# Kernel tuning notes

Measured on AMD Instinct MI355X. Metric: run time of the kernel, lower is better.

## Reference

```python
import jax, jax.numpy as jnp
import numpy as np

HIST, CNTX, PRED = 336, 168, 24
C = 1            # c_in == c_out == 1 (univariate)
HID = 128        # GRU hidden size
NFEAT = 5        # hourly time features (freq_map['H'])
EMB = 10 * NFEAT # embedding_dim * freq_map['H'] = 50
NLAGS = HIST - CNTX            # 168 lag taps
IN_DIM = EMB + NLAGS           # rnn input size = 218
NSAMP = 8192     # num_parallel_samples


def setup_inputs() -> dict:
    key = jax.random.key(0)
    ks = jax.random.split(key, 8)
    s = lambda fan: 1.0 / np.sqrt(fan)
    return {
        "x": jax.random.normal(ks[0], (1, HIST, C), jnp.float32),
        "x_mark": jax.random.normal(ks[1], (1, HIST, NFEAT), jnp.float32),
        "y_mark": jax.random.normal(ks[2], (1, PRED, NFEAT), jnp.float32),
        "W_emb": jax.random.normal(ks[3], (NFEAT, EMB), jnp.float32) * s(NFEAT),
        "b_emb": jnp.zeros((EMB,), jnp.float32),
        "W_ih": jax.random.normal(ks[4], (3 * HID, IN_DIM), jnp.float32) * s(IN_DIM),
        "W_hh": jax.random.normal(ks[5], (3 * HID, HID), jnp.float32) * s(HID),
        "b_ih": jnp.zeros((3 * HID,), jnp.float32),
        "b_hh": jnp.zeros((3 * HID,), jnp.float32),
        "W_proj": jax.random.normal(ks[6], (HID, 3), jnp.float32) * s(HID),
        "b_proj": jnp.zeros((3,), jnp.float32),
        "mode": 0,
    }


def reference(x, x_mark, y_mark, W_emb, b_emb, W_ih, W_hh, b_ih, b_hh, W_proj, b_proj, mode):

    def gru_step(h, xt):  # PyTorch GRU cell semantics (gate order r,z,n)
        gi = xt @ W_ih.T + b_ih
        gh = h @ W_hh.T + b_hh
        i_r, i_z, i_n = jnp.split(gi, 3, axis=-1)
        h_r, h_z, h_n = jnp.split(gh, 3, axis=-1)
        r = jax.nn.sigmoid(i_r + h_r)
        z = jax.nn.sigmoid(i_z + h_z)
        n = jnp.tanh(i_n + r * h_n)
        return (1.0 - z) * n + z * h

    B = x.shape[0]  # 1
    # ----- unroll_encoder (y=None path) -----
    # mean_abs_scaling over last cntx_len steps
    scale = jnp.clip(jnp.mean(jnp.abs(x[:, -CNTX:, :]), axis=1, keepdims=True), 1e-5, None)  # (B,1,C)
    xs = x / scale  # scaled sequence (lags/scale == lags of scaled sequence)
    # lagged subsequences: lag indices 1..NLAGS, subsequence length CNTX
    t_idx = (HIST - CNTX) + jnp.arange(CNTX)[:, None] - jnp.arange(1, NLAGS + 1)[None, :]  # (CNTX, NLAGS)
    lags = xs[:, t_idx, 0]  # (B, CNTX, NLAGS)  (C==1 so flatten is trivial)
    tf = x_mark[:, HIST - CNTX:, :] @ W_emb + b_emb  # (B, CNTX, EMB)
    enc_in = jnp.concatenate([lags, tf], axis=-1)  # (B, CNTX, IN_DIM)
    h0 = jnp.zeros((B, HID), x.dtype)
    h_last, _ = jax.lax.scan(lambda h, xt: (gru_step(h, xt), None), h0,
                             jnp.swapaxes(enc_in, 0, 1))  # final GRU state (B,HID)

    # ----- sampling_decoder -----
    sc = scale[0, 0, 0]  # scalar (B=1, C=1)
    h = jnp.broadcast_to(h_last, (NSAMP, HID))                       # repeat state over samples
    ym = jnp.broadcast_to(y_mark @ W_emb + b_emb, (NSAMP, PRED, EMB))  # repeated embedded marks
    buf = jnp.broadcast_to(x[0, -NLAGS:, 0], (NSAMP, NLAGS))         # last NLAGS observed values
    key0 = jax.random.key(42)

    def step(carry, ym_k):
        buf, h, key = carry
        key, sk = jax.random.split(key)
        lag_in = buf[:, ::-1] / sc                 # decoder lags: most recent first
        xin = jnp.concatenate([lag_in, ym_k], axis=-1)  # (S, IN_DIM)
        h = gru_step(h, xin)
        p = h @ W_proj + b_proj                    # (S, 3) StudentT arg projection
        df = 2.0 + jax.nn.softplus(p[:, 0])
        loc = p[:, 1]
        sigma = jax.nn.softplus(p[:, 2])
        t = jax.random.t(sk, df, shape=df.shape)
        samp = (loc + sigma * t) * sc              # affine-transformed StudentT sample
        buf = jnp.concatenate([buf[:, 1:], samp[:, None]], axis=1)
        return (buf, h, key), samp

    _, samples = jax.lax.scan(step, (buf, h, key0), jnp.swapaxes(ym, 0, 1))  # (PRED, S)
    return samples.T[:, :, None]  # (num_parallel_samples, pred_len, c_out)
```

## Files before the change

kernel.cpp:

```cpp
#include <hip/hip_runtime.h>
#include <stdint.h>

#define HIST 336
#define CNTX 168
#define PRED 24
#define HID 128
#define NFEAT 5
#define EMB 50
#define NLAGS 168
#define IN_DIM 218
#define NSAMP 8192
#define G3 384

#define WS_XS     0
#define WS_SC     336
#define WS_TF     340
#define WS_YM     8740
#define WS_KEYS   9940
#define WS_ENCGI  10036
#define WS_GISH   74548
#define WS_HLAST  83764
#define WS_WIHT   83892

__device__ __forceinline__ uint32_t rotl32(uint32_t v, int r){ return (v<<r)|(v>>(32-r)); }

__device__ __forceinline__ void threefry(uint32_t k0, uint32_t k1, uint32_t x0, uint32_t x1,
                                         uint32_t &o0, uint32_t &o1){
  uint32_t ks2 = k0 ^ k1 ^ 0x1BD11BDAu;
  x0 += k0; x1 += k1;
#define TFR(a) { x0 += x1; x1 = rotl32(x1,(a)); x1 ^= x0; }
  TFR(13) TFR(15) TFR(26) TFR(6)
  x0 += k1; x1 += ks2 + 1u;
  TFR(17) TFR(29) TFR(16) TFR(24)
  x0 += ks2; x1 += k0 + 2u;
  TFR(13) TFR(15) TFR(26) TFR(6)
  x0 += k0; x1 += k1 + 3u;
  TFR(17) TFR(29) TFR(16) TFR(24)
  x0 += k1; x1 += ks2 + 4u;
  TFR(13) TFR(15) TFR(26) TFR(6)
  x0 += ks2; x1 += k0 + 5u;
#undef TFR
  o0 = x0; o1 = x1;
}


__device__ __forceinline__ void tf_split2(uint32_t k0, uint32_t k1,
                                          uint32_t &a0, uint32_t &a1,
                                          uint32_t &b0, uint32_t &b1){
  threefry(k0,k1, 0u,0u, a0,a1);
  threefry(k0,k1, 0u,1u, b0,b1);
}

__device__ __forceinline__ void tf_split3(uint32_t k0, uint32_t k1,
                                          uint32_t &a0, uint32_t &a1,
                                          uint32_t &b0, uint32_t &b1,
                                          uint32_t &c0, uint32_t &c1){
  threefry(k0,k1, 0u,0u, a0,a1);
  threefry(k0,k1, 0u,1u, b0,b1);
  threefry(k0,k1, 0u,2u, c0,c1);
}

__device__ __forceinline__ uint32_t tf_bits1(uint32_t k0, uint32_t k1){
  uint32_t o0,o1; threefry(k0,k1, 0u,0u, o0,o1); return o0 ^ o1;
}

__device__ __forceinline__ uint32_t tf_bits_at(uint32_t k0, uint32_t k1, uint32_t i){
  uint32_t o0,o1; threefry(k0,k1, 0u,i, o0,o1); return o0 ^ o1;
}

__device__ __forceinline__ float bits_to_f01(uint32_t b){
  return __uint_as_float((b>>9) | 0x3f800000u) - 1.0f;
}

__device__ __forceinline__ float erfinv32(float x){
  float w = -log1pf(-x*x);
  float p;
  if (w < 5.0f){
    w = w - 2.5f;
    p = 2.81022636e-08f;
    p = fmaf(p, w, 3.43273939e-07f);
    p = fmaf(p, w, -3.5233877e-06f);
    p = fmaf(p, w, -4.39150654e-06f);
    p = fmaf(p, w, 0.00021858087f);
    p = fmaf(p, w, -0.00125372503f);
    p = fmaf(p, w, -0.00417768164f);
    p = fmaf(p, w, 0.246640727f);
    p = fmaf(p, w, 1.50140941f);
  } else {
    w = sqrtf(w) - 3.0f;
    p = -0.000200214257f;
    p = fmaf(p, w, 0.000100950558f);
    p = fmaf(p, w, 0.00134934322f);
    p = fmaf(p, w, -0.00367342844f);
    p = fmaf(p, w, 0.00573950773f);
    p = fmaf(p, w, -0.0076224613f);
    p = fmaf(p, w, 0.00943887047f);
    p = fmaf(p, w, 1.00167406f);
    p = fmaf(p, w, 2.83297682f);
  }
  return p*x;
}

__device__ __forceinline__ float normal_from_key(uint32_t k0, uint32_t k1){
  uint32_t b = tf_bits1(k0,k1);
  const float lo = -0.99999994f;
  float f = bits_to_f01(b);
  float u = fmaxf(lo, f*2.0f + lo);
  return 1.41421356f * erfinv32(u);
}

__device__ float gamma_sample(uint32_t k0, uint32_t k1, float alpha){
  float d = __fsub_rn(alpha, 0.33333334f);
  float c = 0.33333334f / sqrtf(d);
  uint32_t ck0,ck1, sb0,sb1;
  tf_split2(k0,k1, ck0,ck1, sb0,sb1);
  float V;
  for(;;){
    uint32_t nk0,nk1, xk0,xk1, uk0,uk1;
    tf_split3(ck0,ck1, nk0,nk1, xk0,xk1, uk0,uk1);
    ck0=nk0; ck1=nk1;
    float x, v;
    do {
      uint32_t xa0,xa1, xb0,xb1;
      tf_split2(xk0,xk1, xa0,xa1, xb0,xb1);
      xk0=xa0; xk1=xa1;
      x = normal_from_key(xb0,xb1);
      v = __fadd_rn(1.0f, __fmul_rn(x, c));
    } while (v <= 0.0f);
    float X  = __fmul_rn(x, x);
    float Vv = __fmul_rn(__fmul_rn(v, v), v);
    float U  = bits_to_f01(tf_bits1(uk0,uk1));
    float t1 = __fsub_rn(1.0f, __fmul_rn(0.0331f, __fmul_rn(X, X)));
    bool cont = (U >= t1);
    if (cont){
      float lhs = logf(U);
      float rhs = __fadd_rn(__fmul_rn(0.5f, X),
                  __fmul_rn(d, __fadd_rn(__fsub_rn(1.0f, Vv), logf(Vv))));
      cont = (lhs >= rhs);
    }
    if (!cont){ V = Vv; break; }
  }
  return d*V;
}

__device__ __forceinline__ float softplus_f(float x){
  float amax = fmaxf(x, 0.0f);
  return amax + log1pf(expf(-fabsf(x)));
}

__global__ __launch_bounds__(256) void k1_prep(const float* __restrict__ x,
                                               const float* __restrict__ xmark,
                                               const float* __restrict__ ymark,
                                               const float* __restrict__ Wemb,
                                               const float* __restrict__ bemb,
                                               float* __restrict__ ws){
  __shared__ float red[256];
  __shared__ float s_sc;
  int t = threadIdx.x;
  float a = 0.f;
  if (t < CNTX) a = fabsf(x[CNTX + t]);
  red[t] = a;
  __syncthreads();
  for(int s=128; s>0; s>>=1){ if(t<s) red[t]+=red[t+s]; __syncthreads(); }
  if (t==0){ s_sc = fmaxf(red[0]/168.0f, 1e-5f); ws[WS_SC]=s_sc; }
  __syncthreads();
  float sc = s_sc;
  for(int i=t; i<HIST; i+=256) ws[WS_XS+i] = x[i]/sc;
  for(int idx=t; idx<CNTX*EMB; idx+=256){
    int tt = idx/EMB, e = idx%EMB;
    float acc = bemb[e];
    for(int f=0; f<NFEAT; f++) acc += xmark[(CNTX+tt)*NFEAT+f]*Wemb[f*EMB+e];
    ws[WS_TF+idx] = acc;
  }
  for(int idx=t; idx<PRED*EMB; idx+=256){
    int kk = idx/EMB, e = idx%EMB;
    float acc = bemb[e];
    for(int f=0; f<NFEAT; f++) acc += ymark[kk*NFEAT+f]*Wemb[f*EMB+e];
    ws[WS_YM+idx] = acc;
  }
  if (t==0){
    uint32_t* kp = reinterpret_cast<uint32_t*>(ws + WS_KEYS);
    uint32_t c0 = 0u, c1 = 42u;
    for(int k=0;k<PRED;k++){
      uint32_t a0,a1,b0,b1;
      tf_split2(c0,c1, a0,a1, b0,b1);
      c0=a0; c1=a1;
      uint32_t n0,n1,g0,g1;
      tf_split2(b0,b1, n0,n1, g0,g1);
      kp[k*4+0]=n0; kp[k*4+1]=n1; kp[k*4+2]=g0; kp[k*4+3]=g1;
    }
  }
}

__global__ __launch_bounds__(256) void k2_gi(const float* __restrict__ Wih,
                                             const float* __restrict__ bih,
                                             const float* __restrict__ bhh,
                                             float* __restrict__ ws){
  int idx = blockIdx.x*256 + threadIdx.x;
  if (idx >= 192*G3) return;
  int t = idx / G3, r = idx % G3;
  const float* wr = Wih + r*IN_DIM;
  const float* xs = ws + WS_XS;
  float acc = bih[r] + (r < 256 ? bhh[r] : 0.0f);
  if (t < CNTX){
    const float* tf = ws + WS_TF + t*EMB;
    for(int j=0;j<NLAGS;j++) acc += wr[j]*xs[CNTX + t - 1 - j];
    for(int e=0;e<EMB;e++)   acc += wr[NLAGS+e]*tf[e];
    ws[WS_ENCGI + t*G3 + r] = acc;
  } else {
    int k = t - CNTX;
    const float* ym = ws + WS_YM + k*EMB;
    for(int e=0;e<EMB;e++)   acc += wr[NLAGS+e]*ym[e];
    for(int i=k;i<NLAGS;i++) acc += wr[i]*xs[HIST-1-i+k];
    ws[WS_GISH + k*G3 + r] = acc;
  }
}

__global__ __launch_bounds__(256) void k2b_wiht(const float* __restrict__ Wih,
                                                float* __restrict__ ws){
  int idx = blockIdx.x*256 + threadIdx.x;
  if (idx >= PRED*G3) return;
  int r = idx / PRED, i = idx % PRED;
  ws[WS_WIHT + i*G3 + r] = Wih[r*IN_DIM + i];
}

__global__ __launch_bounds__(384) void k3_enc(const float* __restrict__ Whh,
                                              const float* __restrict__ bhh,
                                              float* __restrict__ ws){
  __shared__ __align__(16) float h[HID];
  __shared__ float grz[256];
  __shared__ float hnv[HID];
  int r = threadIdx.x;
  float4 w[32];
  const float4* wr = (const float4*)(Whh + r*HID);
  #pragma unroll
  for(int i=0;i<32;i++) w[i] = wr[i];
  float bh = (r>=256)? bhh[r] : 0.0f;
  if (r < HID) h[r] = 0.0f;
  __syncthreads();
  const float* encgi = ws + WS_ENCGI;
  for(int t=0;t<CNTX;t++){
    float acc = 0.f;
    #pragma unroll
    for(int i=0;i<32;i++){
      float4 hv = *(const float4*)&h[4*i];
      float4 ww = w[i];
      acc = fmaf(ww.x,hv.x, fmaf(ww.y,hv.y, fmaf(ww.z,hv.z, fmaf(ww.w,hv.w, acc))));
    }
    if (r < 256) grz[r] = encgi[t*G3+r] + acc;
    else         hnv[r-256] = acc + bh;
    __syncthreads();
    if (r < HID){
      float rr = 1.0f/(1.0f+expf(-grz[r]));
      float zz = 1.0f/(1.0f+expf(-grz[128+r]));
      float inv = encgi[t*G3+256+r];
      float nn = tanhf(inv + rr*hnv[r]);
      h[r] = (1.0f-zz)*nn + zz*h[r];
    }
    __syncthreads();
  }
  if (r < HID) ws[WS_HLAST + r] = h[r];
}

#define SPB 32
#define THR 512
#define HROW 132

__global__ __launch_bounds__(512) void k4_dec(const float* __restrict__ Whh,
                                              const float* __restrict__ bhh,
                                              const float* __restrict__ Wproj,
                                              const float* __restrict__ bproj,
                                              const float* __restrict__ ws,
                                              float* __restrict__ out){
  __shared__ __align__(16) float h[SPB][HROW];
  __shared__ float wT[16*G3];
  __shared__ float shist[SPB][PRED];
  __shared__ float parr[SPB][4];
  __shared__ float wp[HID*3];
  __shared__ float bp[3];
  __shared__ uint32_t skeys[PRED*4];

  int t = threadIdx.x;
  int b = blockIdx.x;
  int lane = t & 63;
  int sp = t >> 6;
  int j0 = lane, j1 = lane + 64;
  int s_base = sp*4;

  float sc = ws[WS_SC];
  const float* gish = ws + WS_GISH;
  const float* wihT = ws + WS_WIHT;

  for(int idx=t; idx<HID*3; idx+=THR) wp[idx] = Wproj[idx];
  if (t < 3) bp[t] = bproj[t];
  if (t < PRED*4) skeys[t] = reinterpret_cast<const uint32_t*>(ws + WS_KEYS)[t];
  {
    float h0 = ws[WS_HLAST + j0], h1 = ws[WS_HLAST + j1];
    #pragma unroll
    for(int ss=0;ss<4;ss++){ h[s_base+ss][j0] = h0; h[s_base+ss][j1] = h1; }
  }
  float bhn0 = bhh[256+j0], bhn1 = bhh[256+j1];
  __syncthreads();

  #pragma unroll 1
  for(int k=0;k<PRED;k++){
    float aR[4][2], aZ[4][2], aHN[4][2], aIN[4][2];
    float g_r0 = gish[k*G3 + j0],      g_r1 = gish[k*G3 + j1];
    float g_z0 = gish[k*G3 + 128+j0],  g_z1 = gish[k*G3 + 128+j1];
    float g_n0 = gish[k*G3 + 256+j0],  g_n1 = gish[k*G3 + 256+j1];
    #pragma unroll
    for(int ss=0;ss<4;ss++){
      aR[ss][0]=g_r0;  aR[ss][1]=g_r1;
      aZ[ss][0]=g_z0;  aZ[ss][1]=g_z1;
      aIN[ss][0]=g_n0; aIN[ss][1]=g_n1;
      aHN[ss][0]=bhn0; aHN[ss][1]=bhn1;
    }
    #pragma unroll 1
    for(int i=0;i<k;i++){
      const float* wrow = wihT + i*G3;
      float w_r0 = wrow[j0],     w_r1 = wrow[j1];
      float w_z0 = wrow[128+j0], w_z1 = wrow[128+j1];
      float w_n0 = wrow[256+j0], w_n1 = wrow[256+j1];
      #pragma unroll
      for(int ss=0;ss<4;ss++){
        float sh = shist[s_base+ss][k-1-i];
        aR[ss][0]  = fmaf(w_r0, sh, aR[ss][0]);  aR[ss][1]  = fmaf(w_r1, sh, aR[ss][1]);
        aZ[ss][0]  = fmaf(w_z0, sh, aZ[ss][0]);  aZ[ss][1]  = fmaf(w_z1, sh, aZ[ss][1]);
        aIN[ss][0] = fmaf(w_n0, sh, aIN[ss][0]); aIN[ss][1] = fmaf(w_n1, sh, aIN[ss][1]);
      }
    }
    #pragma unroll 1
    for(int kt=0; kt<8; kt++){
      __syncthreads();
      #pragma unroll
      for(int i=0;i<3;i++){
        int f4 = t + i*THR;
        int rr = f4 >> 2, c4 = f4 & 3;
        float4 g = *(const float4*)&Whh[rr*HID + kt*16 + c4*4];
        wT[(c4*4+0)*G3 + rr] = g.x;
        wT[(c4*4+1)*G3 + rr] = g.y;
        wT[(c4*4+2)*G3 + rr] = g.z;
        wT[(c4*4+3)*G3 + rr] = g.w;
      }
      __syncthreads();
      #pragma unroll
      for(int c4=0;c4<4;c4++){
        float hx[4], hy[4], hz[4], hw[4];
        #pragma unroll
        for(int ss=0;ss<4;ss++){
          float4 hv = *(const float4*)&h[s_base+ss][kt*16+c4*4];
          hx[ss]=hv.x; hy[ss]=hv.y; hz[ss]=hv.z; hw[ss]=hv.w;
        }
        #pragma unroll
        for(int u=0;u<4;u++){
          const float* wc = &wT[(c4*4+u)*G3];
          float wr0 = wc[j0], wz0 = wc[128+j0], wn0 = wc[256+j0];
          float wr1 = wc[j1], wz1 = wc[128+j1], wn1 = wc[256+j1];
          #pragma unroll
          for(int ss=0;ss<4;ss++){
            float hc = (u==0)?hx[ss]:(u==1)?hy[ss]:(u==2)?hz[ss]:hw[ss];
            aR[ss][0]  = fmaf(wr0, hc, aR[ss][0]);  aR[ss][1]  = fmaf(wr1, hc, aR[ss][1]);
            aZ[ss][0]  = fmaf(wz0, hc, aZ[ss][0]);  aZ[ss][1]  = fmaf(wz1, hc, aZ[ss][1]);
            aHN[ss][0] = fmaf(wn0, hc, aHN[ss][0]); aHN[ss][1] = fmaf(wn1, hc, aHN[ss][1]);
          }
        }
      }
    }
    __syncthreads();
    #pragma unroll
    for(int ss=0;ss<4;ss++){
      int s = s_base+ss;
      {
        float rr = 1.0f/(1.0f+expf(-aR[ss][0]));
        float zz = 1.0f/(1.0f+expf(-aZ[ss][0]));
        float nn = tanhf(aIN[ss][0] + rr*aHN[ss][0]);
        h[s][j0] = (1.0f-zz)*nn + zz*h[s][j0];
      }
      {
        float rr = 1.0f/(1.0f+expf(-aR[ss][1]));
        float zz = 1.0f/(1.0f+expf(-aZ[ss][1]));
        float nn = tanhf(aIN[ss][1] + rr*aHN[ss][1]);
        h[s][j1] = (1.0f-zz)*nn + zz*h[s][j1];
      }
    }
    __syncthreads();
    if (t < SPB*3){
      int s = t/3, c2 = t%3;
      float acc = bp[c2];
      for(int l=0;l<HID;l++) acc = fmaf(h[s][l], wp[l*3+c2], acc);
      parr[s][c2] = acc;
    }
    __syncthreads();
    if (t < SPB){
      int s = t, gs = b*SPB + s;
      float p0 = parr[s][0], loc = parr[s][1], p2 = parr[s][2];
      float df = 2.0f + softplus_f(p0);
      float half_df = df*0.5f;
      float sigma = softplus_f(p2);
      uint32_t kn0 = skeys[k*4+0], kn1 = skeys[k*4+1];
      uint32_t kg0 = skeys[k*4+2], kg1 = skeys[k*4+3];
      uint32_t bnb = tf_bits_at(kn0, kn1, (uint32_t)gs);
      const float lo = -0.99999994f;
      float un = fmaxf(lo, bits_to_f01(bnb)*2.0f + lo);
      float nval = 1.41421356f * erfinv32(un);
      uint32_t gk0, gk1;
      threefry(kg0, kg1, 0u, (uint32_t)gs, gk0, gk1);
      float g = gamma_sample(gk0, gk1, half_df);
      float tval = nval * sqrtf(half_df / g);
      float samp = (loc + sigma*tval)*sc;
      out[gs*PRED + k] = samp;
      shist[s][k] = samp / sc;
    }
    __syncthreads();
  }
}

extern "C" void kernel_launch(void* const* d_in, const int* in_sizes, int n_in,
                              void* d_out, int out_size, void* d_ws, size_t ws_size,
                              hipStream_t stream){
  const float* x     = (const float*)d_in[0];
  const float* xmark = (const float*)d_in[1];
  const float* ymark = (const float*)d_in[2];
  const float* Wemb  = (const float*)d_in[3];
  const float* bemb  = (const float*)d_in[4];
  const float* Wih   = (const float*)d_in[5];
  const float* Whh   = (const float*)d_in[6];
  const float* bih   = (const float*)d_in[7];
  const float* bhh   = (const float*)d_in[8];
  const float* Wproj = (const float*)d_in[9];
  const float* bproj = (const float*)d_in[10];
  float* ws  = (float*)d_ws;
  float* out = (float*)d_out;

  hipLaunchKernelGGL(k1_prep, dim3(1), dim3(256), 0, stream, x, xmark, ymark, Wemb, bemb, ws);
  hipLaunchKernelGGL(k2_gi, dim3(288), dim3(256), 0, stream, Wih, bih, bhh, ws);
  hipLaunchKernelGGL(k2b_wiht, dim3((PRED*G3+255)/256), dim3(256), 0, stream, Wih, ws);
  hipLaunchKernelGGL(k3_enc, dim3(1), dim3(384), 0, stream, Whh, bhh, ws);
  hipLaunchKernelGGL(k4_dec, dim3(NSAMP/SPB), dim3(THR), 0, stream, Whh, bhh, Wproj, bproj, ws, out);
}
```

Measured before the change: 845.3 us.

## Double-buffer W_hh tiles in decoder with register-staged prefetch and larger K chunk

After: 805.5 us. -4.7%, faster.

```diff
diff --git a/kernel.cpp b/kernel.cpp
--- a/kernel.cpp
+++ b/kernel.cpp
@@ -42,7 +42,6 @@
 #undef TFR
   o0 = x0; o1 = x1;
 }
-
 
 __device__ __forceinline__ void tf_split2(uint32_t k0, uint32_t k1,
                                           uint32_t &a0, uint32_t &a1,
@@ -265,6 +264,8 @@
 #define SPB 32
 #define THR 512
 #define HROW 132
+#define BK 32
+#define G3P 385
 
 __global__ __launch_bounds__(512) void k4_dec(const float* __restrict__ Whh,
                                               const float* __restrict__ bhh,
@@ -272,8 +273,8 @@
                                               const float* __restrict__ bproj,
                                               const float* __restrict__ ws,
                                               float* __restrict__ out){
+  __shared__ __align__(16) float wT[2][BK*G3P];
   __shared__ __align__(16) float h[SPB][HROW];
-  __shared__ float wT[16*G3];
   __shared__ float shist[SPB][PRED];
   __shared__ float parr[SPB][4];
   __shared__ float wp[HID*3];
@@ -300,7 +301,19 @@
     for(int ss=0;ss<4;ss++){ h[s_base+ss][j0] = h0; h[s_base+ss][j1] = h1; }
   }
   float bhn0 = bhh[256+j0], bhn1 = bhh[256+j1];
+
+  #pragma unroll
+  for(int i=0;i<6;i++){
+    int f4 = i*THR + t;
+    int rr = f4 >> 3, q = f4 & 7;
+    float4 g = *(const float4*)&Whh[rr*HID + q*4];
+    wT[0][(q*4+0)*G3P + rr] = g.x;
+    wT[0][(q*4+1)*G3P + rr] = g.y;
+    wT[0][(q*4+2)*G3P + rr] = g.z;
+    wT[0][(q*4+3)*G3P + rr] = g.w;
+  }
   __syncthreads();
+  int p = 0;
 
   #pragma unroll 1
   for(int k=0;k<PRED;k++){
@@ -330,32 +343,31 @@
       }
     }
     #pragma unroll 1
-    for(int kt=0; kt<8; kt++){
-      __syncthreads();
+    for(int c=0;c<4;c++){
+      int cn = (c+1)&3;
+      float4 stg[6];
+      int srr[6], sq[6];
       #pragma unroll
-      for(int i=0;i<3;i++){
-        int f4 = t + i*THR;
-        int rr = f4 >> 2, c4 = f4 & 3;
-        float4 g = *(const float4*)&Whh[rr*HID + kt*16 + c4*4];
-        wT[(c4*4+0)*G3 + rr] = g.x;
-        wT[(c4*4+1)*G3 + rr] = g.y;
-        wT[(c4*4+2)*G3 + rr] = g.z;
-        wT[(c4*4+3)*G3 + rr] = g.w;
-      }
-      __syncthreads();
+      for(int i=0;i<6;i++){
+        int f4 = i*THR + t;
+        srr[i] = f4 >> 3; sq[i] = f4 & 7;
+        stg[i] = *(const float4*)&Whh[srr[i]*HID + cn*BK + sq[i]*4];
+      }
+      const float* wcur = wT[p];
       #pragma unroll
-      for(int c4=0;c4<4;c4++){
+      for(int kq=0;kq<8;kq++){
         float hx[4], hy[4], hz[4], hw[4];
         #pragma unroll
         for(int ss=0;ss<4;ss++){
-          float4 hv = *(const float4*)&h[s_base+ss][kt*16+c4*4];
+          float4 hv = *(const float4*)&h[s_base+ss][c*BK + kq*4];
           hx[ss]=hv.x; hy[ss]=hv.y; hz[ss]=hv.z; hw[ss]=hv.w;
         }
         #pragma unroll
         for(int u=0;u<4;u++){
-          const float* wc = &wT[(c4*4+u)*G3];
-          float wr0 = wc[j0], wz0 = wc[128+j0], wn0 = wc[256+j0];
-          float wr1 = wc[j1], wz1 = wc[128+j1], wn1 = wc[256+j1];
+          const float* wc = wcur + (kq*4+u)*G3P;
+          float wr0 = wc[j0],     wr1 = wc[j0+64];
+          float wz0 = wc[j0+128], wz1 = wc[j0+192];
+          float wn0 = wc[j0+256], wn1 = wc[j0+320];
           #pragma unroll
           for(int ss=0;ss<4;ss++){
             float hc = (u==0)?hx[ss]:(u==1)?hy[ss]:(u==2)?hz[ss]:hw[ss];
@@ -365,8 +377,17 @@
           }
         }
       }
-    }
-    __syncthreads();
+      float* wnx = wT[p^1];
+      #pragma unroll
+      for(int i=0;i<6;i++){
+        wnx[(sq[i]*4+0)*G3P + srr[i]] = stg[i].x;
+        wnx[(sq[i]*4+1)*G3P + srr[i]] = stg[i].y;
+        wnx[(sq[i]*4+2)*G3P + srr[i]] = stg[i].z;
+        wnx[(sq[i]*4+3)*G3P + srr[i]] = stg[i].w;
+      }
+      __syncthreads();
+      p ^= 1;
+    }
     #pragma unroll
     for(int ss=0;ss<4;ss++){
       int s = s_base+ss;
```

## Keep W_hh rows in registers, one gate row per thread in decoder

Applied to the files above, without the earlier changes.

New measurement: 1.951 ms. 2.31x slower.

```diff
diff --git a/kernel.cpp b/kernel.cpp
--- a/kernel.cpp
+++ b/kernel.cpp
@@ -42,7 +42,6 @@
 #undef TFR
   o0 = x0; o1 = x1;
 }
-
 
 __device__ __forceinline__ void tf_split2(uint32_t k0, uint32_t k1,
                                           uint32_t &a0, uint32_t &a1,
@@ -263,137 +262,115 @@
 }
 
 #define SPB 32
-#define THR 512
-#define HROW 132
-
-__global__ __launch_bounds__(512) void k4_dec(const float* __restrict__ Whh,
-                                              const float* __restrict__ bhh,
-                                              const float* __restrict__ Wproj,
-                                              const float* __restrict__ bproj,
-                                              const float* __restrict__ ws,
-                                              float* __restrict__ out){
-  __shared__ __align__(16) float h[SPB][HROW];
-  __shared__ float wT[16*G3];
-  __shared__ float shist[SPB][PRED];
-  __shared__ float parr[SPB][4];
+#define THR4 384
+
+__global__ __launch_bounds__(384, 2) void k4_dec(const float* __restrict__ Whh,
+                                                 const float* __restrict__ bhh,
+                                                 const float* __restrict__ Wproj,
+                                                 const float* __restrict__ bproj,
+                                                 const float* __restrict__ ws,
+                                                 float* __restrict__ out){
+  __shared__ float g[512][33];
+  __shared__ float h[SPB][129];
+  __shared__ float wihT_l[24*G3];
+  __shared__ float shist[SPB][25];
   __shared__ float wp[HID*3];
   __shared__ float bp[3];
   __shared__ uint32_t skeys[PRED*4];
 
   int t = threadIdx.x;
   int b = blockIdx.x;
-  int lane = t & 63;
-  int sp = t >> 6;
-  int j0 = lane, j1 = lane + 64;
-  int s_base = sp*4;
-
+  int r = t;
+
+  float4 w[32];
+  {
+    const float4* wr = (const float4*)(Whh + r*HID);
+    #pragma unroll
+    for(int i=0;i<32;i++) w[i] = wr[i];
+  }
+  float bhn = (r >= 256) ? bhh[r] : 0.0f;
+
+  for(int idx=t; idx<24*G3; idx+=THR4) wihT_l[idx] = ws[WS_WIHT + idx];
+  for(int idx=t; idx<HID*3; idx+=THR4) wp[idx] = Wproj[idx];
+  if (t < 3) bp[t] = bproj[t];
+  if (t < PRED*4) skeys[t] = reinterpret_cast<const uint32_t*>(ws + WS_KEYS)[t];
+  if (t < HID){
+    float hl = ws[WS_HLAST + t];
+    for(int s=0;s<SPB;s++) h[s][t] = hl;
+  }
   float sc = ws[WS_SC];
   const float* gish = ws + WS_GISH;
-  const float* wihT = ws + WS_WIHT;
-
-  for(int idx=t; idx<HID*3; idx+=THR) wp[idx] = Wproj[idx];
-  if (t < 3) bp[t] = bproj[t];
-  if (t < PRED*4) skeys[t] = reinterpret_cast<const uint32_t*>(ws + WS_KEYS)[t];
-  {
-    float h0 = ws[WS_HLAST + j0], h1 = ws[WS_HLAST + j1];
-    #pragma unroll
-    for(int ss=0;ss<4;ss++){ h[s_base+ss][j0] = h0; h[s_base+ss][j1] = h1; }
-  }
-  float bhn0 = bhh[256+j0], bhn1 = bhh[256+j1];
   __syncthreads();
 
   #pragma unroll 1
   for(int k=0;k<PRED;k++){
-    float aR[4][2], aZ[4][2], aHN[4][2], aIN[4][2];
-    float g_r0 = gish[k*G3 + j0],      g_r1 = gish[k*G3 + j1];
-    float g_z0 = gish[k*G3 + 128+j0],  g_z1 = gish[k*G3 + 128+j1];
-    float g_n0 = gish[k*G3 + 256+j0],  g_n1 = gish[k*G3 + 256+j1];
-    #pragma unroll
-    for(int ss=0;ss<4;ss++){
-      aR[ss][0]=g_r0;  aR[ss][1]=g_r1;
-      aZ[ss][0]=g_z0;  aZ[ss][1]=g_z1;
-      aIN[ss][0]=g_n0; aIN[ss][1]=g_n1;
-      aHN[ss][0]=bhn0; aHN[ss][1]=bhn1;
-    }
+    float gk_init = gish[k*G3 + r];
     #pragma unroll 1
-    for(int i=0;i<k;i++){
-      const float* wrow = wihT + i*G3;
-      float w_r0 = wrow[j0],     w_r1 = wrow[j1];
-      float w_z0 = wrow[128+j0], w_z1 = wrow[128+j1];
-      float w_n0 = wrow[256+j0], w_n1 = wrow[256+j1];
-      #pragma unroll
-      for(int ss=0;ss<4;ss++){
-        float sh = shist[s_base+ss][k-1-i];
-        aR[ss][0]  = fmaf(w_r0, sh, aR[ss][0]);  aR[ss][1]  = fmaf(w_r1, sh, aR[ss][1]);
-        aZ[ss][0]  = fmaf(w_z0, sh, aZ[ss][0]);  aZ[ss][1]  = fmaf(w_z1, sh, aZ[ss][1]);
-        aIN[ss][0] = fmaf(w_n0, sh, aIN[ss][0]); aIN[ss][1] = fmaf(w_n1, sh, aIN[ss][1]);
+    for(int sg=0; sg<8; sg++){
+      int s0 = sg*4;
+      float a0=gk_init, a1=gk_init, a2=gk_init, a3=gk_init;
+      float c0=bhn, c1=bhn, c2=bhn, c3=bhn;
+      #pragma unroll 1
+      for(int i=0;i<k;i++){
+        float wv = wihT_l[i*G3 + r];
+        a0 = fmaf(wv, shist[s0+0][k-1-i], a0);
+        a1 = fmaf(wv, shist[s0+1][k-1-i], a1);
+        a2 = fmaf(wv, shist[s0+2][k-1-i], a2);
+        a3 = fmaf(wv, shist[s0+3][k-1-i], a3);
       }
-    }
-    #pragma unroll 1
-    for(int kt=0; kt<8; kt++){
-      __syncthreads();
-      #pragma unroll
-      for(int i=0;i<3;i++){
-        int f4 = t + i*THR;
-        int rr = f4 >> 2, c4 = f4 & 3;
-        float4 g = *(const float4*)&Whh[rr*HID + kt*16 + c4*4];
-        wT[(c4*4+0)*G3 + rr] = g.x;
-        wT[(c4*4+1)*G3 + rr] = g.y;
-        wT[(c4*4+2)*G3 + rr] = g.z;
-        wT[(c4*4+3)*G3 + rr] = g.w;
+      if (r < 256){
+        #pragma unroll
+        for(int q=0;q<32;q++){
+          float4 h0 = *(const float4*)&h[s0+0][q*4];
+          float4 h1 = *(const float4*)&h[s0+1][q*4];
+          float4 h2 = *(const float4*)&h[s0+2][q*4];
+          float4 h3 = *(const float4*)&h[s0+3][q*4];
+          float4 ww = w[q];
+          a0 = fmaf(ww.x,h0.x,a0); a1 = fmaf(ww.x,h1.x,a1); a2 = fmaf(ww.x,h2.x,a2); a3 = fmaf(ww.x,h3.x,a3);
+          a0 = fmaf(ww.y,h0.y,a0); a1 = fmaf(ww.y,h1.y,a1); a2 = fmaf(ww.y,h2.y,a2); a3 = fmaf(ww.y,h3.y,a3);
+          a0 = fmaf(ww.z,h0.z,a0); a1 = fmaf(ww.z,h1.z,a1); a2 = fmaf(ww.z,h2.z,a2); a3 = fmaf(ww.z,h3.z,a3);
+          a0 = fmaf(ww.w,h0.w,a0); a1 = fmaf(ww.w,h1.w,a1); a2 = fmaf(ww.w,h2.w,a2); a3 = fmaf(ww.w,h3.w,a3);
+        }
+        g[r][s0+0]=a0; g[r][s0+1]=a1; g[r][s0+2]=a2; g[r][s0+3]=a3;
+      } else {
+        #pragma unroll
+        for(int q=0;q<32;q++){
+          float4 h0 = *(const float4*)&h[s0+0][q*4];
+          float4 h1 = *(const float4*)&h[s0+1][q*4];
+          float4 h2 = *(const float4*)&h[s0+2][q*4];
+          float4 h3 = *(const float4*)&h[s0+3][q*4];
+          float4 ww = w[q];
+          c0 = fmaf(ww.x,h0.x,c0); c1 = fmaf(ww.x,h1.x,c1); c2 = fmaf(ww.x,h2.x,c2); c3 = fmaf(ww.x,h3.x,c3);
+          c0 = fmaf(ww.y,h0.y,c0); c1 = fmaf(ww.y,h1.y,c1); c2 = fmaf(ww.y,h2.y,c2); c3 = fmaf(ww.y,h3.y,c3);
+          c0 = fmaf(ww.z,h0.z,c0); c1 = fmaf(ww.z,h1.z,c1); c2 = fmaf(ww.z,h2.z,c2); c3 = fmaf(ww.z,h3.z,c3);
+          c0 = fmaf(ww.w,h0.w,c0); c1 = fmaf(ww.w,h1.w,c1); c2 = fmaf(ww.w,h2.w,c2); c3 = fmaf(ww.w,h3.w,c3);
+        }
+        g[r][s0+0]=a0; g[r][s0+1]=a1; g[r][s0+2]=a2; g[r][s0+3]=a3;
+        g[r+128][s0+0]=c0; g[r+128][s0+1]=c1; g[r+128][s0+2]=c2; g[r+128][s0+3]=c3;
       }
-      __syncthreads();
-      #pragma unroll
-      for(int c4=0;c4<4;c4++){
-        float hx[4], hy[4], hz[4], hw[4];
-        #pragma unroll
-        for(int ss=0;ss<4;ss++){
-          float4 hv = *(const float4*)&h[s_base+ss][kt*16+c4*4];
-          hx[ss]=hv.x; hy[ss]=hv.y; hz[ss]=hv.z; hw[ss]=hv.w;
-        }
-        #pragma unroll
-        for(int u=0;u<4;u++){
-          const float* wc = &wT[(c4*4+u)*G3];
-          float wr0 = wc[j0], wz0 = wc[128+j0], wn0 = wc[256+j0];
-          float wr1 = wc[j1], wz1 = wc[128+j1], wn1 = wc[256+j1];
-          #pragma unroll
-          for(int ss=0;ss<4;ss++){
-            float hc = (u==0)?hx[ss]:(u==1)?hy[ss]:(u==2)?hz[ss]:hw[ss];
-            aR[ss][0]  = fmaf(wr0, hc, aR[ss][0]);  aR[ss][1]  = fmaf(wr1, hc, aR[ss][1]);
-            aZ[ss][0]  = fmaf(wz0, hc, aZ[ss][0]);  aZ[ss][1]  = fmaf(wz1, hc, aZ[ss][1]);
-            aHN[ss][0] = fmaf(wn0, hc, aHN[ss][0]); aHN[ss][1] = fmaf(wn1, hc, aHN[ss][1]);
-          }
-        }
+    }
+    __syncthreads();
+    {
+      int j = t & 127, sgrp = t >> 7;
+      for(int s=sgrp; s<SPB; s+=3){
+        float aRv = g[j][s], aZv = g[128+j][s], aINv = g[256+j][s], aHNv = g[384+j][s];
+        float rr = 1.0f/(1.0f+expf(-aRv));
+        float zz = 1.0f/(1.0f+expf(-aZv));
+        float nn = tanhf(aINv + rr*aHNv);
+        h[s][j] = (1.0f-zz)*nn + zz*h[s][j];
       }
-    }
-    __syncthreads();
-    #pragma unroll
-    for(int ss=0;ss<4;ss++){
-      int s = s_base+ss;
-      {
-        float rr = 1.0f/(1.0f+expf(-aR[ss][0]));
-        float zz = 1.0f/(1.0f+expf(-aZ[ss][0]));
-        float nn = tanhf(aIN[ss][0] + rr*aHN[ss][0]);
-        h[s][j0] = (1.0f-zz)*nn + zz*h[s][j0];
-      }
-      {
-        float rr = 1.0f/(1.0f+expf(-aR[ss][1]));
-        float zz = 1.0f/(1.0f+expf(-aZ[ss][1]));
-        float nn = tanhf(aIN[ss][1] + rr*aHN[ss][1]);
-        h[s][j1] = (1.0f-zz)*nn + zz*h[s][j1];
-      }
-    }
-    __syncthreads();
-    if (t < SPB*3){
-      int s = t/3, c2 = t%3;
-      float acc = bp[c2];
-      for(int l=0;l<HID;l++) acc = fmaf(h[s][l], wp[l*3+c2], acc);
-      parr[s][c2] = acc;
     }
     __syncthreads();
     if (t < SPB){
       int s = t, gs = b*SPB + s;
-      float p0 = parr[s][0], loc = parr[s][1], p2 = parr[s][2];
+      float p0 = bp[0], p1 = bp[1], p2 = bp[2];
+      for(int l=0;l<HID;l++){
+        float hv = h[s][l];
+        p0 = fmaf(hv, wp[l*3+0], p0);
+        p1 = fmaf(hv, wp[l*3+1], p1);
+        p2 = fmaf(hv, wp[l*3+2], p2);
+      }
+      float loc = p1;
       float df = 2.0f + softplus_f(p0);
       float half_df = df*0.5f;
       float sigma = softplus_f(p2);
@@ -405,8 +382,8 @@
       float nval = 1.41421356f * erfinv32(un);
       uint32_t gk0, gk1;
       threefry(kg0, kg1, 0u, (uint32_t)gs, gk0, gk1);
-      float g = gamma_sample(gk0, gk1, half_df);
-      float tval = nval * sqrtf(half_df / g);
+      float gmm = gamma_sample(gk0, gk1, half_df);
+      float tval = nval * sqrtf(half_df / gmm);
       float samp = (loc + sigma*tval)*sc;
       out[gs*PRED + k] = samp;
       shist[s][k] = samp / sc;
@@ -436,5 +413,5 @@
   hipLaunchKernelGGL(k2_gi, dim3(288), dim3(256), 0, stream, Wih, bih, bhh, ws);
   hipLaunchKernelGGL(k2b_wiht, dim3((PRED*G3+255)/256), dim3(256), 0, stream, Wih, ws);
   hipLaunchKernelGGL(k3_enc, dim3(1), dim3(384), 0, stream, Whh, bhh, ws);
-  hipLaunchKernelGGL(k4_dec, dim3(NSAMP/SPB), dim3(THR), 0, stream, Whh, bhh, Wproj, bproj, ws, out);
-}
+  hipLaunchKernelGGL(k4_dec, dim3(NSAMP/SPB), dim3(THR4), 0, stream, Whh, bhh, Wproj, bproj, ws, out);
+}
```
